# Kernel tuning notes

Measured on AMD Instinct MI355X. Metric: run time of the kernel, lower is better.

## Reference

```python
import jax, jax.numpy as jnp
import numpy as np

DIMBED = 1024
DIMLAT = 1024
SEQ = 2048
BATCH = 16
LN_EPS = float(DIMBED)  # quirk: nn.LayerNorm(BATCH_SIZE, dimbed) -> eps = dimbed


def setup_inputs() -> dict:
    key = jax.random.key(0)
    ks = jax.random.split(key, 8)
    s_in = 1.0 / np.sqrt(DIMBED)
    s_lat = 1.0 / np.sqrt(DIMLAT)
    return {
        "x": jax.random.normal(ks[0], (SEQ, DIMBED, BATCH), dtype=jnp.float32),
        "Wq": jax.random.normal(ks[1], (DIMLAT, DIMBED), dtype=jnp.float32) * s_in,
        "Wk": jax.random.normal(ks[2], (DIMLAT, DIMBED), dtype=jnp.float32) * s_in,
        "Wv": jax.random.normal(ks[3], (DIMLAT, DIMBED), dtype=jnp.float32) * s_in,
        "Wg": jax.random.normal(ks[4], (DIMBED, DIMLAT), dtype=jnp.float32) * s_lat,
        "bg": jax.random.normal(ks[5], (DIMBED,), dtype=jnp.float32) * 0.01,
        "ln_w": jnp.ones((BATCH,), dtype=jnp.float32),
        "ln_b": jnp.zeros((BATCH,), dtype=jnp.float32),
    }


def reference(x, Wq, Wk, Wv, Wg, bg, ln_w, ln_b):
    # LayerNorm over last axis (size BATCH=16), eps = dimbed (faithful quirk)
    mu = jnp.mean(x, axis=-1, keepdims=True)
    var = jnp.mean(jnp.square(x - mu), axis=-1, keepdims=True)
    xt = (x - mu) * jax.lax.rsqrt(var + LN_EPS) * ln_w + ln_b  # (S, D, B)

    xt2 = jnp.transpose(xt, (0, 2, 1))  # (S, B, D) -- x.transpose(1,2)
    q = jnp.einsum('sbd,ld->sbl', xt2, Wq)  # (S, B, L)
    k = jnp.einsum('sbd,ld->sbl', xt2, Wk)
    v = jnp.einsum('sbd,ld->sbl', xt2, Wv)

    # e[b,s,t] = sum_l q[s,b,l] * k[t,b,l]
    e = jnp.einsum('sbl,tbl->bst', q, k)  # (B, S, S)
    # softmax over dim=1 (the query axis s), scaled by 1/sqrt(dimbed)
    a = jax.nn.softmax(e / np.sqrt(DIMBED).astype(np.float32), axis=1)
    ftheta = jnp.einsum('bst,tbl->bsl', a, v)  # (B, S, L)

    out = jnp.einsum('bsl,dl->bsd', ftheta, Wg) + bg  # (B, S, D)
    return jnp.transpose(out, (1, 2, 0))  # (S, D, B)
```

## Files before the change

### kernel.cpp

```cpp
#include <hip/hip_runtime.h>
#include <hip/hip_bf16.h>
#include <stdint.h>

using bf16 = __hip_bfloat16;
typedef __attribute__((ext_vector_type(4))) float f32x4;
typedef __attribute__((ext_vector_type(8))) short s16x8;
typedef __attribute__((ext_vector_type(4))) short s16x4;

#define SEQN 2048
#define DIMD 1024
#define NB   16

#define GLDS16(gp, lp)                                                      \
  __builtin_amdgcn_global_load_lds(                                         \
      (const __attribute__((address_space(1))) void*)(gp),                  \
      (__attribute__((address_space(3))) void*)(lp), 16, 0, 0)

__global__ void cvt_kernel(const float* __restrict__ Wq, const float* __restrict__ Wk,
                           const float* __restrict__ Wv, const float* __restrict__ Wg,
                           bf16* __restrict__ Wqkv, bf16* __restrict__ Wgb) {
  const int i = blockIdx.x * 256 + threadIdx.x;
  const int which = blockIdx.y;
  const float* src = (which == 0) ? Wq : (which == 1) ? Wk : (which == 2) ? Wv : Wg;
  bf16* dst = (which < 3) ? (Wqkv + (size_t)which * DIMD * DIMD) : Wgb;
  f32x4 f = ((const f32x4*)src)[i];
  s16x4 pack;
#pragma unroll
  for (int j = 0; j < 4; ++j) {
    bf16 t = __float2bfloat16(f[j]);
    pack[j] = *reinterpret_cast<short*>(&t);
  }
  *reinterpret_cast<s16x4*>(dst + (size_t)i * 4) = pack;
}

__global__ void ln_kernel(const float* __restrict__ x, const float* __restrict__ lnw,
                          const float* __restrict__ lnb, bf16* __restrict__ xt) {
  const int idx = blockIdx.x * 256 + threadIdx.x;
  const int s = idx >> 10, d = idx & 1023;
  const float4* xp = reinterpret_cast<const float4*>(x + (size_t)idx * NB);
  float v[16];
#pragma unroll
  for (int j = 0; j < 4; ++j) reinterpret_cast<float4*>(v)[j] = xp[j];
  float mu = 0.f;
#pragma unroll
  for (int j = 0; j < 16; ++j) mu += v[j];
  mu *= (1.f / 16.f);
  float var = 0.f;
#pragma unroll
  for (int j = 0; j < 16; ++j) { float t = v[j] - mu; var += t * t; }
  var *= (1.f / 16.f);
  const float inv = rsqrtf(var + 1024.0f);
#pragma unroll
  for (int b = 0; b < 16; ++b) {
    float o = (v[b] - mu) * inv * lnw[b] + lnb[b];
    xt[((size_t)b * SEQN + s) * DIMD + d] = __float2bfloat16(o);
  }
}

template <int MODE>
__global__ __launch_bounds__(512, 2)
void gemm256(const bf16* __restrict__ Ag, const bf16* __restrict__ Bg,
             bf16* __restrict__ C, float* __restrict__ Cf,
             const float* __restrict__ bias,
             const int K, const int lda, const int ldb, const size_t ldc,
             const size_t sA, const size_t sB, const size_t sC,
             const int tn, const float escale) {
  __shared__ bf16 sm[2][2][16384];

  const int nwg = gridDim.x;
  const int flat = blockIdx.x;
  const int tile = (flat & 7) * (nwg >> 3) + (flat >> 3);
  const int m0 = (tile / tn) * 256;
  const int n0 = (tile % tn) * 256;

  const int bz = blockIdx.z;
  const bf16* A = Ag + (size_t)bz * sA;
  const bf16* B = Bg + (size_t)bz * sB;
  const size_t coff = (size_t)bz * sC;

  const int tid = threadIdx.x;
  const int w = tid >> 6;
  const int lane = tid & 63;
  const int wr = w >> 2, wc = w & 3;
  const int r16 = lane & 15, hi = lane >> 4;
  const int xorb = r16 & 7;

  const int slrow = tid >> 3;
  const int sgrp = (tid & 7) ^ (slrow & 7);
  const bf16* gSA = A + (size_t)(m0 + slrow) * lda + sgrp * 8;
  const bf16* gSB = B + (size_t)(n0 + slrow) * ldb + sgrp * 8;
  const int w512 = w * 512;

  const int off0 = r16 * 64 + ((0 + hi) ^ xorb) * 8;
  const int off1 = r16 * 64 + ((4 + hi) ^ xorb) * 8;

  f32x4 acc[8][4] = {};
  s16x8 aF[4][2], bF[2][2];
  const int NT = K >> 6;

#define SQ_A(q, kt, bb)                                                      \
  GLDS16(gSA + (size_t)((q) * 64) * lda + (size_t)(kt) * 64,                 \
         &sm[bb][0][(q) * 4096 + w512])
#define SQ_B(q, kt, bb)                                                      \
  GLDS16(gSB + (size_t)((q) * 64) * ldb + (size_t)(kt) * 64,                 \
         &sm[bb][1][(q) * 4096 + w512])

#define READ_A(mh, bb) do {                                                  \
    const bf16* pa_ = &sm[bb][0][(2 * wr + (mh)) * 4096];                    \
    _Pragma("unroll")                                                        \
    for (int sub = 0; sub < 4; ++sub) {                                      \
      aF[sub][0] = *(const s16x8*)(pa_ + sub * 1024 + off0);                 \
      aF[sub][1] = *(const s16x8*)(pa_ + sub * 1024 + off1);                 \
    }                                                                        \
  } while (0)

#define READ_B(nh, bb) do {                                                  \
    const bf16* pb_ = &sm[bb][1][wc * 4096 + (nh) * 2048];                   \
    _Pragma("unroll")                                                        \
    for (int j = 0; j < 2; ++j) {                                            \
      bF[j][0] = *(const s16x8*)(pb_ + j * 1024 + off0);                     \
      bF[j][1] = *(const s16x8*)(pb_ + j * 1024 + off1);                     \
    }                                                                        \
  } while (0)

#define MFMA_Q(mh, nh) do {                                                  \
    __builtin_amdgcn_s_setprio(1);                                           \
    _Pragma("unroll")                                                        \
    for (int k = 0; k < 2; ++k)                                              \
      _Pragma("unroll")                                                      \
      for (int j = 0; j < 2; ++j)                                            \
        _Pragma("unroll")                                                    \
        for (int sub = 0; sub < 4; ++sub)                                    \
          acc[(mh) * 4 + sub][(nh) * 2 + j] = __builtin_amdgcn_mfma_f32_16x16x32_bf16( \
              aF[sub][k], bF[j][k], acc[(mh) * 4 + sub][(nh) * 2 + j], 0, 0, 0); \
    __builtin_amdgcn_s_setprio(0);                                           \
  } while (0)

#define BAR() asm volatile("s_barrier" ::: "memory")
#define VMW(n) asm volatile("s_waitcnt vmcnt(" #n ")" ::: "memory")

  SQ_B(0, 0, 0); SQ_B(1, 0, 0); SQ_B(2, 0, 0); SQ_B(3, 0, 0);
  SQ_A(0, 0, 0); SQ_A(2, 0, 0); SQ_A(1, 0, 0); SQ_A(3, 0, 0);
  VMW(2);
  BAR();

  int t = 0;
  for (; t < NT - 1; ++t) {
    const int cb = t & 1, nb = cb ^ 1, nk = t + 1;
    READ_A(0, cb); READ_B(0, cb);
    SQ_B(0, nk, nb); SQ_B(1, nk, nb);
    BAR(); MFMA_Q(0, 0); BAR();
    READ_B(1, cb);
    SQ_B(2, nk, nb); SQ_B(3, nk, nb);
    VMW(4);
    BAR(); MFMA_Q(0, 1); BAR();
    READ_A(1, cb); READ_B(0, cb);
    SQ_A(0, nk, nb); SQ_A(2, nk, nb);
    BAR(); MFMA_Q(1, 0); BAR();
    READ_B(1, cb);
    SQ_A(1, nk, nb); SQ_A(3, nk, nb);
    VMW(2);
    BAR(); MFMA_Q(1, 1); BAR();
  }
  {
    const int cb = t & 1;
    READ_A(0, cb); READ_B(0, cb); BAR(); MFMA_Q(0, 0); BAR();
    READ_B(1, cb); VMW(0); BAR(); MFMA_Q(0, 1); BAR();
    READ_A(1, cb); READ_B(0, cb); BAR(); MFMA_Q(1, 0); BAR();
    READ_B(1, cb); BAR(); MFMA_Q(1, 1); BAR();
  }

#undef SQ_A
#undef SQ_B
#undef READ_A
#undef READ_B
#undef MFMA_Q
#undef BAR
#undef VMW

#pragma unroll
  for (int mf = 0; mf < 8; ++mf) {
#pragma unroll
    for (int nf = 0; nf < 4; ++nf) {
      f32x4 v = acc[mf][nf];
      const int gm0 = m0 + wr * 128 + mf * 16 + hi * 4;
      const int gn = n0 + wc * 64 + nf * 16 + r16;
#pragma unroll
      for (int i = 0; i < 4; ++i) {
        const int gm = gm0 + i;
        if (MODE == 0) {
          C[coff + (size_t)gm * ldc + gn] = __float2bfloat16(v[i]);
        } else if (MODE == 1) {
          C[coff + (size_t)gm * ldc + gn] = __float2bfloat16(__expf(v[i] * escale));
        } else {
          Cf[((size_t)(gm >> 4)) * (DIMD * NB) + (size_t)gn * NB + (gm & 15)] = v[i] + bias[gn];
        }
      }
    }
  }
}

__global__ void colsum_kernel(const bf16* __restrict__ p, float* __restrict__ Zp) {
  const int tcol = blockIdx.x * 256 + threadIdx.x;
  const int b = blockIdx.y;
  const int ch = blockIdx.z;
  const bf16* pp = p + ((size_t)b * SEQN + ch * 256) * SEQN + tcol;
  float s = 0.f;
#pragma unroll 8
  for (int i = 0; i < 256; ++i) s += __bfloat162float(pp[(size_t)i * SEQN]);
  Zp[((size_t)ch * NB + b) * SEQN + tcol] = s;
}

__global__ void zinv_kernel(const float* __restrict__ Zp, float* __restrict__ Zinv) {
  const int i = blockIdx.x * 256 + threadIdx.x;
  float s = 0.f;
#pragma unroll
  for (int c = 0; c < 8; ++c) s += Zp[(size_t)c * (NB * SEQN) + i];
  Zinv[i] = 1.0f / s;
}

__global__ void vtrans_kernel(const bf16* __restrict__ QKV, const float* __restrict__ Zinv,
                              bf16* __restrict__ vpp) {
  __shared__ bf16 tile[64][66];
  const int b = blockIdx.z;
  const int t0 = blockIdx.x * 64;
  const int l0 = blockIdx.y * 64;
  const int tid = threadIdx.x;
  const int col = tid & 63, rw = tid >> 6;
#pragma unroll
  for (int i = 0; i < 16; ++i) {
    const int r = i * 4 + rw;
    tile[r][col] = QKV[((size_t)b * SEQN + t0 + r) * 3072 + 2048 + l0 + col];
  }
  __syncthreads();
  const float z = Zinv[b * SEQN + t0 + col];
#pragma unroll
  for (int i = 0; i < 16; ++i) {
    const int lr = i * 4 + rw;
    vpp[((size_t)b * DIMD + l0 + lr) * SEQN + t0 + col] =
        __float2bfloat16(__bfloat162float(tile[col][lr]) * z);
  }
}

extern "C" void kernel_launch(void* const* d_in, const int* in_sizes, int n_in,
                              void* d_out, int out_size, void* d_ws, size_t ws_size,
                              hipStream_t stream) {
  const float* x   = (const float*)d_in[0];
  const float* Wq  = (const float*)d_in[1];
  const float* Wk  = (const float*)d_in[2];
  const float* Wv  = (const float*)d_in[3];
  const float* Wg  = (const float*)d_in[4];
  const float* bg  = (const float*)d_in[5];
  const float* lnw = (const float*)d_in[6];
  const float* lnb = (const float*)d_in[7];
  float* out = (float*)d_out;

  char* ws = (char*)d_ws;
  size_t off = 0;
  auto alloc = [&](size_t bytes) {
    char* p = ws + off;
    off += (bytes + 255) & ~(size_t)255;
    return p;
  };
  bf16* Wqkv = (bf16*)alloc((size_t)3072 * DIMD * 2);
  bf16* Wgb  = (bf16*)alloc((size_t)DIMD * DIMD * 2);
  bf16* xt   = (bf16*)alloc((size_t)NB * SEQN * DIMD * 2);
  bf16* QKV  = (bf16*)alloc((size_t)NB * SEQN * 3072 * 2);
  bf16* p    = (bf16*)alloc((size_t)NB * SEQN * SEQN * 2);
  float* Zp  = (float*)alloc((size_t)8 * NB * SEQN * 4);
  float* Zinv = (float*)alloc((size_t)NB * SEQN * 4);
  bf16* vpp = xt;
  bf16* fth = QKV;

  const dim3 blk(256);
  const dim3 blk512(512);

  cvt_kernel<<<dim3(1024, 4), blk, 0, stream>>>(Wq, Wk, Wv, Wg, Wqkv, Wgb);
  ln_kernel<<<dim3(SEQN * DIMD / 256), blk, 0, stream>>>(x, lnw, lnb, xt);
  gemm256<0><<<dim3(128 * 12, 1, 1), blk512, 0, stream>>>(
      xt, Wqkv, QKV, nullptr, nullptr,
       DIMD,  DIMD,  DIMD,  3072,
      0, 0, 0,  12, 0.f);
  gemm256<1><<<dim3(8 * 8, 1, 16), blk512, 0, stream>>>(
      QKV, QKV + 1024, p, nullptr, nullptr,
       DIMD,  3072,  3072,  SEQN,
      (size_t)SEQN * 3072, (size_t)SEQN * 3072, (size_t)SEQN * SEQN,  8, 0.03125f);
  colsum_kernel<<<dim3(8, 16, 8), blk, 0, stream>>>(p, Zp);
  zinv_kernel<<<dim3(NB * SEQN / 256), blk, 0, stream>>>(Zp, Zinv);
  vtrans_kernel<<<dim3(32, 16, 16), blk, 0, stream>>>(QKV, Zinv, vpp);
  gemm256<0><<<dim3(8 * 4, 1, 16), blk512, 0, stream>>>(
      p, vpp, fth, nullptr, nullptr,
       SEQN,  SEQN,  SEQN,  (size_t)NB * DIMD,
      (size_t)SEQN * SEQN, (size_t)DIMD * SEQN, DIMD,  4, 0.f);
  gemm256<2><<<dim3(128 * 4, 1, 1), blk512, 0, stream>>>(
      fth, Wgb, nullptr, out, bg,
       DIMD,  DIMD,  DIMD,  0,
      0, 0, 0,  4, 0.f);
}
```

Before: 860.3 us.

## Fuse softmax column sums into QK GEMM epilogue and restructure B-fragment loads

```diff
diff --git a/kernel.cpp b/kernel.cpp
--- a/kernel.cpp
+++ b/kernel.cpp
@@ -95,7 +95,7 @@
   const int off1 = r16 * 64 + ((4 + hi) ^ xorb) * 8;
 
   f32x4 acc[8][4] = {};
-  s16x8 aF[4][2], bF[2][2];
+  s16x8 aF[4][2], bF[4][2];
   const int NT = K >> 6;
 
 #define SQ_A(q, kt, bb)                                                      \
@@ -114,10 +114,10 @@
     }                                                                        \
   } while (0)
 
-#define READ_B(nh, bb) do {                                                  \
-    const bf16* pb_ = &sm[bb][1][wc * 4096 + (nh) * 2048];                   \
+#define READ_B_ALL(bb) do {                                                  \
+    const bf16* pb_ = &sm[bb][1][wc * 4096];                                 \
     _Pragma("unroll")                                                        \
-    for (int j = 0; j < 2; ++j) {                                            \
+    for (int j = 0; j < 4; ++j) {                                            \
       bF[j][0] = *(const s16x8*)(pb_ + j * 1024 + off0);                     \
       bF[j][1] = *(const s16x8*)(pb_ + j * 1024 + off1);                     \
     }                                                                        \
@@ -132,7 +132,7 @@
         _Pragma("unroll")                                                    \
         for (int sub = 0; sub < 4; ++sub)                                    \
           acc[(mh) * 4 + sub][(nh) * 2 + j] = __builtin_amdgcn_mfma_f32_16x16x32_bf16( \
-              aF[sub][k], bF[j][k], acc[(mh) * 4 + sub][(nh) * 2 + j], 0, 0, 0); \
+              aF[sub][k], bF[(nh) * 2 + j][k], acc[(mh) * 4 + sub][(nh) * 2 + j], 0, 0, 0); \
     __builtin_amdgcn_s_setprio(0);                                           \
   } while (0)
 
@@ -147,37 +147,34 @@
   int t = 0;
   for (; t < NT - 1; ++t) {
     const int cb = t & 1, nb = cb ^ 1, nk = t + 1;
-    READ_A(0, cb); READ_B(0, cb);
-    SQ_B(0, nk, nb); SQ_B(1, nk, nb);
+    READ_B_ALL(cb); READ_A(0, cb);
+    SQ_B(0, nk, nb); SQ_B(1, nk, nb); SQ_B(2, nk, nb); SQ_B(3, nk, nb);
     BAR(); MFMA_Q(0, 0); BAR();
-    READ_B(1, cb);
-    SQ_B(2, nk, nb); SQ_B(3, nk, nb);
-    VMW(4);
+    SQ_A(0, nk, nb); SQ_A(2, nk, nb); SQ_A(1, nk, nb); SQ_A(3, nk, nb);
+    VMW(8);
     BAR(); MFMA_Q(0, 1); BAR();
-    READ_A(1, cb); READ_B(0, cb);
-    SQ_A(0, nk, nb); SQ_A(2, nk, nb);
+    READ_A(1, cb);
     BAR(); MFMA_Q(1, 0); BAR();
-    READ_B(1, cb);
-    SQ_A(1, nk, nb); SQ_A(3, nk, nb);
     VMW(2);
     BAR(); MFMA_Q(1, 1); BAR();
   }
   {
     const int cb = t & 1;
-    READ_A(0, cb); READ_B(0, cb); BAR(); MFMA_Q(0, 0); BAR();
-    READ_B(1, cb); VMW(0); BAR(); MFMA_Q(0, 1); BAR();
-    READ_A(1, cb); READ_B(0, cb); BAR(); MFMA_Q(1, 0); BAR();
-    READ_B(1, cb); BAR(); MFMA_Q(1, 1); BAR();
+    READ_B_ALL(cb); READ_A(0, cb); BAR(); MFMA_Q(0, 0); BAR();
+    VMW(0); BAR(); MFMA_Q(0, 1); BAR();
+    READ_A(1, cb); BAR(); MFMA_Q(1, 0);
+    MFMA_Q(1, 1);
   }
 
 #undef SQ_A
 #undef SQ_B
 #undef READ_A
-#undef READ_B
+#undef READ_B_ALL
 #undef MFMA_Q
 #undef BAR
 #undef VMW
 
+  float cs[4] = {0.f, 0.f, 0.f, 0.f};
 #pragma unroll
   for (int mf = 0; mf < 8; ++mf) {
 #pragma unroll
@@ -191,35 +188,32 @@
         if (MODE == 0) {
           C[coff + (size_t)gm * ldc + gn] = __float2bfloat16(v[i]);
         } else if (MODE == 1) {
-          C[coff + (size_t)gm * ldc + gn] = __float2bfloat16(__expf(v[i] * escale));
+          const float e = __expf(v[i] * escale);
+          C[coff + (size_t)gm * ldc + gn] = __float2bfloat16(e);
+          cs[nf] += e;
         } else {
           Cf[((size_t)(gm >> 4)) * (DIMD * NB) + (size_t)gn * NB + (gm & 15)] = v[i] + bias[gn];
         }
       }
     }
   }
-}
-
-__global__ void colsum_kernel(const bf16* __restrict__ p, float* __restrict__ Zp) {
-  const int tcol = blockIdx.x * 256 + threadIdx.x;
-  const int b = blockIdx.y;
-  const int ch = blockIdx.z;
-  const bf16* pp = p + ((size_t)b * SEQN + ch * 256) * SEQN + tcol;
-  float s = 0.f;
-#pragma unroll 8
-  for (int i = 0; i < 256; ++i) s += __bfloat162float(pp[(size_t)i * SEQN]);
-  Zp[((size_t)ch * NB + b) * SEQN + tcol] = s;
-}
-
-__global__ void zinv_kernel(const float* __restrict__ Zp, float* __restrict__ Zinv) {
-  const int i = blockIdx.x * 256 + threadIdx.x;
-  float s = 0.f;
-#pragma unroll
-  for (int c = 0; c < 8; ++c) s += Zp[(size_t)c * (NB * SEQN) + i];
-  Zinv[i] = 1.0f / s;
-}
-
-__global__ void vtrans_kernel(const bf16* __restrict__ QKV, const float* __restrict__ Zinv,
+  if (MODE == 1) {
+#pragma unroll
+    for (int nf = 0; nf < 4; ++nf) {
+      cs[nf] += __shfl_xor(cs[nf], 16);
+      cs[nf] += __shfl_xor(cs[nf], 32);
+    }
+    if (hi == 0) {
+#pragma unroll
+      for (int nf = 0; nf < 4; ++nf) {
+        const int gn = n0 + wc * 64 + nf * 16 + r16;
+        atomicAdd(&Cf[(size_t)bz * SEQN + gn], cs[nf]);
+      }
+    }
+  }
+}
+
+__global__ void vtrans_kernel(const bf16* __restrict__ QKV, const float* __restrict__ Zsum,
                               bf16* __restrict__ vpp) {
   __shared__ bf16 tile[64][66];
   const int b = blockIdx.z;
@@ -233,7 +227,7 @@
     tile[r][col] = QKV[((size_t)b * SEQN + t0 + r) * 3072 + 2048 + l0 + col];
   }
   __syncthreads();
-  const float z = Zinv[b * SEQN + t0 + col];
+  const float z = 1.0f / Zsum[b * SEQN + t0 + col];
 #pragma unroll
   for (int i = 0; i < 16; ++i) {
     const int lr = i * 4 + rw;
@@ -267,8 +261,7 @@
   bf16* xt   = (bf16*)alloc((size_t)NB * SEQN * DIMD * 2);
   bf16* QKV  = (bf16*)alloc((size_t)NB * SEQN * 3072 * 2);
   bf16* p    = (bf16*)alloc((size_t)NB * SEQN * SEQN * 2);
-  float* Zp  = (float*)alloc((size_t)8 * NB * SEQN * 4);
-  float* Zinv = (float*)alloc((size_t)NB * SEQN * 4);
+  float* Zsum = (float*)alloc((size_t)NB * SEQN * 4);
   bf16* vpp = xt;
   bf16* fth = QKV;
 
@@ -277,17 +270,16 @@
 
   cvt_kernel<<<dim3(1024, 4), blk, 0, stream>>>(Wq, Wk, Wv, Wg, Wqkv, Wgb);
   ln_kernel<<<dim3(SEQN * DIMD / 256), blk, 0, stream>>>(x, lnw, lnb, xt);
+  hipMemsetAsync(Zsum, 0, (size_t)NB * SEQN * 4, stream);
   gemm256<0><<<dim3(128 * 12, 1, 1), blk512, 0, stream>>>(
       xt, Wqkv, QKV, nullptr, nullptr,
        DIMD,  DIMD,  DIMD,  3072,
       0, 0, 0,  12, 0.f);
   gemm256<1><<<dim3(8 * 8, 1, 16), blk512, 0, stream>>>(
-      QKV, QKV + 1024, p, nullptr, nullptr,
+      QKV, QKV + 1024, p, Zsum, nullptr,
        DIMD,  3072,  3072,  SEQN,
       (size_t)SEQN * 3072, (size_t)SEQN * 3072, (size_t)SEQN * SEQN,  8, 0.03125f);
-  colsum_kernel<<<dim3(8, 16, 8), blk, 0, stream>>>(p, Zp);
-  zinv_kernel<<<dim3(NB * SEQN / 256), blk, 0, stream>>>(Zp, Zinv);
-  vtrans_kernel<<<dim3(32, 16, 16), blk, 0, stream>>>(QKV, Zinv, vpp);
+  vtrans_kernel<<<dim3(32, 16, 16), blk, 0, stream>>>(QKV, Zsum, vpp);
   gemm256<0><<<dim3(8 * 4, 1, 16), blk512, 0, stream>>>(
       p, vpp, fth, nullptr, nullptr,
        SEQN,  SEQN,  SEQN,  (size_t)NB * DIMD,
```

Result: no change. 847.1 us (-1.5%).
